# Kernel tuning notes

Measured on AMD Instinct MI355X. Metric: run time of the kernel, lower is better.

Reference implementation:

```python
import jax, jax.numpy as jnp
import numpy as np

N_NODES = 100000
N_EDGES = 3200000
IN_C = 128
OUT_C = 40
NEG_SLOPE = 0.2


def _p(key, shape, scale=0.1):
    return jax.random.normal(key, shape, dtype=jnp.float32) * scale


def setup_inputs() -> dict:
    key = jax.random.key(0)
    ks = jax.random.split(key, 16)
    x = jax.random.normal(ks[0], (N_NODES, IN_C), dtype=jnp.float32)
    edge_index = jax.random.randint(ks[1], (2, N_EDGES), 0, N_NODES, dtype=jnp.int32)
    # layer 1: in=128 -> heads=4, out=4 (concat -> 16)
    W1 = _p(ks[2], (IN_C, 4 * 4))
    a_src1 = _p(ks[3], (4, 4))
    a_dst1 = _p(ks[4], (4, 4))
    b1 = jnp.zeros((16,), jnp.float32)
    # layer 2: 16 -> heads=8, out=8 (concat -> 64)
    W2 = _p(ks[5], (16, 8 * 8))
    a_src2 = _p(ks[6], (8, 8))
    a_dst2 = _p(ks[7], (8, 8))
    b2 = jnp.zeros((64,), jnp.float32)
    # layer 3: 64 -> heads=1, out=OUT_C, concat=False
    W3 = _p(ks[8], (64, OUT_C))
    a_src3 = _p(ks[9], (1, OUT_C))
    a_dst3 = _p(ks[10], (1, OUT_C))
    b3 = jnp.zeros((OUT_C,), jnp.float32)
    return {"x": x, "edge_index": edge_index,
            "W1": W1, "a_src1": a_src1, "a_dst1": a_dst1, "b1": b1,
            "W2": W2, "a_src2": a_src2, "a_dst2": a_dst2, "b2": b2,
            "W3": W3, "a_src3": a_src3, "a_dst3": a_dst3, "b3": b3}


def gat_conv(x, src, dst, W, a_src, a_dst, b, heads, out_c, concat):
    # x: [N, F_in]; src/dst: [E] (self loops already included)
    N = x.shape[0]
    h = (x @ W).reshape(N, heads, out_c)                 # [N, H, C]
    e_src = jnp.sum(h * a_src, axis=-1)                  # [N, H]
    e_dst = jnp.sum(h * a_dst, axis=-1)                  # [N, H]
    e = jax.nn.leaky_relu(e_src[src] + e_dst[dst], NEG_SLOPE)  # [E, H]
    # segment softmax over edges grouped by destination node
    m = jax.ops.segment_max(e, dst, num_segments=N)      # [N, H]
    ex = jnp.exp(e - m[dst])
    s = jax.ops.segment_sum(ex, dst, num_segments=N)
    alpha = ex / (s[dst] + 1e-16)                        # [E, H]
    out = jax.ops.segment_sum(h[src] * alpha[:, :, None], dst, num_segments=N)  # [N, H, C]
    out = out.reshape(N, heads * out_c) if concat else out.mean(axis=1)
    return out + b


def reference(x, edge_index, W1, a_src1, a_dst1, b1, W2, a_src2, a_dst2, b2, W3, a_src3, a_dst3, b3):
    N = x.shape[0]
    loops = jnp.arange(N, dtype=edge_index.dtype)
    src = jnp.concatenate([edge_index[0], loops])
    dst = jnp.concatenate([edge_index[1], loops])
    h = jax.nn.elu(gat_conv(x, src, dst, W1, a_src1, a_dst1, b1, 4, 4, True))
    h = jax.nn.elu(gat_conv(h, src, dst, W2, a_src2, a_dst2, b2, 8, 8, True))
    out = gat_conv(h, src, dst, W3, a_src3, a_dst3, b3, 1, OUT_C, False)
    return out
```

## Files before the change

### kernel.cpp

```cpp
#include <hip/hip_runtime.h>

#define NN 100000
#define NE 3200000
#define ET (NE + NN)
#define NEG_SLOPE 0.2f
#define BSH 8
#define WIN (1 << BSH)
#define NBUC ((NN + WIN - 1) >> BSH)
#define NBLK 256
#define EPB ((ET + NBLK - 1) / NBLK)

__device__ __host__ __forceinline__ int swz(int b) {
    return (b & 7) * (NBLK / 8) + (b >> 3);
}

__device__ __forceinline__ float lrelu(float v) { return v > 0.f ? v : NEG_SLOPE * v; }

__device__ __forceinline__ unsigned short f2bf(float x) {
    unsigned u = __float_as_uint(x);
    return (unsigned short)((u + 0x7fffu + ((u >> 16) & 1u)) >> 16);
}
__device__ __forceinline__ float bflo(unsigned u) { return __uint_as_float(u << 16); }
__device__ __forceinline__ float bfhi(unsigned u) { return __uint_as_float(u & 0xffff0000u); }

typedef float f32x2 __attribute__((ext_vector_type(2)));
__device__ __forceinline__ f32x2 pkfma(f32x2 a, f32x2 b, f32x2 c) {
#if __has_builtin(__builtin_elementwise_fma)
    return __builtin_elementwise_fma(a, b, c);
#else
    f32x2 r; r.x = fmaf(a.x, b.x, c.x); r.y = fmaf(a.y, b.y, c.y); return r;
#endif
}
__device__ __forceinline__ f32x2 bfpair(unsigned u) {
    f32x2 r; r.x = bflo(u); r.y = bfhi(u); return r;
}


template <int FIN, int FOUT, int C>
__device__ __forceinline__ void gemm_attn_body(
    int idx, const float* __restrict__ x, const float* Ws,
    const float* __restrict__ a_src, const float* __restrict__ a_dst,
    unsigned short* __restrict__ h, float* __restrict__ esrc,
    float* __restrict__ edst, int N) {
    constexpr int HH = FOUT / C;
    constexpr int F4 = FOUT / 4;
    constexpr int TPH = C / 4;
    if (idx >= N * F4) return;
    int n = idx / F4, f4 = idx - n * F4;
    int fb = 4 * f4;
    const float4* xr = (const float4*)(x + (long)n * FIN);
    float a0 = 0.f, a1 = 0.f, a2 = 0.f, a3 = 0.f;
#pragma unroll
    for (int k4 = 0; k4 < FIN / 4; ++k4) {
        float4 xv = xr[k4];
        const float* wr = &Ws[(4 * k4) * FOUT + fb];
        float4 w0 = *(const float4*)(wr);
        float4 w1 = *(const float4*)(wr + FOUT);
        float4 w2 = *(const float4*)(wr + 2 * FOUT);
        float4 w3 = *(const float4*)(wr + 3 * FOUT);
        a0 = fmaf(xv.x, w0.x, a0); a1 = fmaf(xv.x, w0.y, a1);
        a2 = fmaf(xv.x, w0.z, a2); a3 = fmaf(xv.x, w0.w, a3);
        a0 = fmaf(xv.y, w1.x, a0); a1 = fmaf(xv.y, w1.y, a1);
        a2 = fmaf(xv.y, w1.z, a2); a3 = fmaf(xv.y, w1.w, a3);
        a0 = fmaf(xv.z, w2.x, a0); a1 = fmaf(xv.z, w2.y, a1);
        a2 = fmaf(xv.z, w2.z, a2); a3 = fmaf(xv.z, w2.w, a3);
        a0 = fmaf(xv.w, w3.x, a0); a1 = fmaf(xv.w, w3.y, a1);
        a2 = fmaf(xv.w, w3.z, a2); a3 = fmaf(xv.w, w3.w, a3);
    }
    unsigned short b0 = f2bf(a0), b1 = f2bf(a1), b2 = f2bf(a2), b3 = f2bf(a3);
    *(ushort4*)(h + (long)n * FOUT + fb) = make_ushort4(b0, b1, b2, b3);
    float q0 = bflo((unsigned)b0), q1 = bflo((unsigned)b1);
    float q2 = bflo((unsigned)b2), q3 = bflo((unsigned)b3);
    float vs = q0 * a_src[fb] + q1 * a_src[fb + 1] + q2 * a_src[fb + 2] + q3 * a_src[fb + 3];
    float vd = q0 * a_dst[fb] + q1 * a_dst[fb + 1] + q2 * a_dst[fb + 2] + q3 * a_dst[fb + 3];
#pragma unroll
    for (int o = 1; o < TPH; o <<= 1) {
        vs += __shfl_xor(vs, o);
        vd += __shfl_xor(vd, o);
    }
    if ((f4 % TPH) == 0) {
        int hh = f4 / TPH;
        esrc[n * HH + hh] = vs;
        edst[n * HH + hh] = vd;
    }
}


__global__ __launch_bounds__(256) void cntgemm_kernel(
    const int* __restrict__ dst, int* __restrict__ cnt,
    const float* __restrict__ x, const float* __restrict__ W,
    const float* __restrict__ a_src, const float* __restrict__ a_dst,
    unsigned short* __restrict__ h, float* __restrict__ esrc,
    float* __restrict__ edst, int N) {
    __shared__ __align__(16) char smem[128 * 16 * 4];
    if (blockIdx.x < NBLK) {
        int* hh = (int*)smem;
        for (int i = threadIdx.x; i < NBUC; i += 256) hh[i] = 0;
        __syncthreads();
        int lo = blockIdx.x * EPB;
        int hi = lo + EPB; if (hi > ET) hi = ET;
        for (int k = lo + threadIdx.x; k < hi; k += 256) {
            int d = (k < NE) ? dst[k] : k - NE;
            atomicAdd(&hh[d >> BSH], 1);
        }
        __syncthreads();
        int col = swz(blockIdx.x);
        for (int i = threadIdx.x; i < NBUC; i += 256)
            cnt[i * NBLK + col] = hh[i];
    } else {
        float* Ws = (float*)smem;
        for (int i = threadIdx.x; i < 128 * 16; i += 256) Ws[i] = W[i];
        __syncthreads();
        int idx = (blockIdx.x - NBLK) * 256 + threadIdx.x;
        gemm_attn_body<128, 16, 4>(idx, x, Ws, a_src, a_dst, h, esrc, edst, N);
    }
}


__global__ __launch_bounds__(256) void rowsum_kernel(const int* __restrict__ cnt,
                                                     int* __restrict__ tot) {
    int wave = threadIdx.x >> 6, lane = threadIdx.x & 63;
    int b = blockIdx.x * 4 + wave;
    if (b >= NBUC) return;
    int4 v = ((const int4*)(cnt + b * NBLK))[lane];
    int s = v.x + v.y + v.z + v.w;
#pragma unroll
    for (int off = 32; off; off >>= 1) s += __shfl_xor(s, off);
    if (lane == 0) tot[b] = s;
}

__global__ __launch_bounds__(1024) void scan_kernel(const int* __restrict__ tot,
                                                    int* __restrict__ bstart) {
    __shared__ int t[1024];
    int b = threadIdx.x;
    int s = (b < NBUC) ? tot[b] : 0;
    t[b] = s;
    __syncthreads();
    for (int off = 1; off < 1024; off <<= 1) {
        int v = (b >= off) ? t[b - off] : 0;
        __syncthreads();
        t[b] += v;
        __syncthreads();
    }
    if (b < NBUC) bstart[b] = t[b] - s;
    if (b == 0) bstart[NBUC] = ET;
}

__global__ __launch_bounds__(256) void base_kernel(int* __restrict__ cnt,
                                                   const int* __restrict__ bstart) {
    int wave = threadIdx.x >> 6, lane = threadIdx.x & 63;
    int b = blockIdx.x * 4 + wave;
    if (b >= NBUC) return;
    int run = bstart[b];
    for (int c0 = 0; c0 < NBLK; c0 += 64) {
        int v = cnt[b * NBLK + c0 + lane];
        int x = v;
#pragma unroll
        for (int off = 1; off < 64; off <<= 1) {
            int y = __shfl_up(x, off);
            if (lane >= off) x += y;
        }
        cnt[b * NBLK + c0 + lane] = run + x - v;
        run += __shfl(x, 63);
    }
}

__global__ __launch_bounds__(1024) void scatter_kernel(const int* __restrict__ src,
                                                       const int* __restrict__ dst,
                                                       const int* __restrict__ base,
                                                       unsigned* __restrict__ tmpp) {
    __shared__ int loff[NBUC];
    int col = swz(blockIdx.x);
    for (int i = threadIdx.x; i < NBUC; i += 1024) loff[i] = base[i * NBLK + col];
    __syncthreads();
    int lo = blockIdx.x * EPB;
    int hi = lo + EPB; if (hi > ET) hi = ET;
    for (int k = lo + threadIdx.x; k < hi; k += 1024) {
        int s, d;
        if (k < NE) { s = src[k]; d = dst[k]; }
        else { s = d = k - NE; }
        int p = atomicAdd(&loff[d >> BSH], 1);
        tmpp[p] = (unsigned)s | ((unsigned)(d & (WIN - 1)) << 17);
    }
}

__global__ __launch_bounds__(1024) void sort_kernel(const int* __restrict__ bstart,
                                                    const unsigned* __restrict__ tmpp,
                                                    int* __restrict__ rowptr,
                                                    int* __restrict__ ssrc) {
    __shared__ int histw[16][WIN];
    __shared__ int scan[WIN];
    __shared__ int cur[WIN];
    int buc = blockIdx.x;
    int nlo = buc << BSH;
    int nwin = NN - nlo; if (nwin > WIN) nwin = WIN;
    int lo = bstart[buc], hi = bstart[buc + 1];
    int tid = threadIdx.x;
    int wv = tid >> 6;
    for (int i = tid; i < 16 * WIN; i += 1024) ((int*)histw)[i] = 0;
    __syncthreads();
    for (int k = lo + tid; k < hi; k += 1024)
        atomicAdd(&histw[wv][tmpp[k] >> 17], 1);
    __syncthreads();
    int myh = 0;
    if (tid < WIN) {
        int s = 0;
#pragma unroll
        for (int w = 0; w < 16; ++w) s += histw[w][tid];
        myh = s;
        scan[tid] = s;
    }
    __syncthreads();
    for (int off = 1; off < WIN; off <<= 1) {
        int v = (tid >= off && tid < WIN) ? scan[tid - off] : 0;
        __syncthreads();
        if (tid < WIN) scan[tid] += v;
        __syncthreads();
    }
    if (tid < WIN) {
        int ex = scan[tid] - myh;
        cur[tid] = ex;
        if (tid < nwin) rowptr[nlo + tid] = lo + ex;
    }
    if (buc == 0 && tid == 0) rowptr[NN] = ET;
    __syncthreads();
    for (int k = lo + tid; k < hi; k += 1024) {
        unsigned e = tmpp[k];
        int p = atomicAdd(&cur[e >> 17], 1);
        ssrc[lo + p] = (int)(e & 0x1FFFFu);
    }
}


template <int FIN, int FOUT, int C>
__global__ __launch_bounds__(256) void gemm_attn_kernel(
    const float* __restrict__ x, const float* __restrict__ W,
    const float* __restrict__ a_src, const float* __restrict__ a_dst,
    unsigned short* __restrict__ h, float* __restrict__ esrc,
    float* __restrict__ edst, int N) {
    __shared__ __align__(16) float Ws[FIN * FOUT];
    for (int i = threadIdx.x; i < FIN * FOUT; i += blockDim.x) Ws[i] = W[i];
    __syncthreads();
    int idx = blockIdx.x * blockDim.x + threadIdx.x;
    gemm_attn_body<FIN, FOUT, C>(idx, x, Ws, a_src, a_dst, h, esrc, edst, N);
}

__global__ __launch_bounds__(320) void gemm_attn3_kernel(
    const float* __restrict__ x, const float* __restrict__ W,
    const float* __restrict__ a_src, const float* __restrict__ a_dst,
    unsigned short* __restrict__ h, float* __restrict__ esrc,
    float* __restrict__ edst, int N) {
    constexpr int FIN = 64, FOUT = 40, F4 = 10;
    __shared__ __align__(16) float Ws[FIN * FOUT];
    __shared__ float ps[320], pd[320];
    int tid = threadIdx.x;
    for (int i = tid; i < FIN * FOUT; i += 320) Ws[i] = W[i];
    __syncthreads();
    int idx = blockIdx.x * 320 + tid;
    int n = idx / F4, f4 = idx - n * F4;
    float vs = 0.f, vd = 0.f;
    if (n < N) {
        int fb = 4 * f4;
        const float4* xr = (const float4*)(x + (long)n * FIN);
        float a0 = 0.f, a1 = 0.f, a2 = 0.f, a3 = 0.f;
#pragma unroll
        for (int k4 = 0; k4 < FIN / 4; ++k4) {
            float4 xv = xr[k4];
            const float* wr = &Ws[(4 * k4) * FOUT + fb];
            float4 w0 = *(const float4*)(wr);
            float4 w1 = *(const float4*)(wr + FOUT);
            float4 w2 = *(const float4*)(wr + 2 * FOUT);
            float4 w3 = *(const float4*)(wr + 3 * FOUT);
            a0 = fmaf(xv.x, w0.x, a0); a1 = fmaf(xv.x, w0.y, a1);
            a2 = fmaf(xv.x, w0.z, a2); a3 = fmaf(xv.x, w0.w, a3);
            a0 = fmaf(xv.y, w1.x, a0); a1 = fmaf(xv.y, w1.y, a1);
            a2 = fmaf(xv.y, w1.z, a2); a3 = fmaf(xv.y, w1.w, a3);
            a0 = fmaf(xv.z, w2.x, a0); a1 = fmaf(xv.z, w2.y, a1);
            a2 = fmaf(xv.z, w2.z, a2); a3 = fmaf(xv.z, w2.w, a3);
            a0 = fmaf(xv.w, w3.x, a0); a1 = fmaf(xv.w, w3.y, a1);
            a2 = fmaf(xv.w, w3.z, a2); a3 = fmaf(xv.w, w3.w, a3);
        }
        unsigned short b0 = f2bf(a0), b1 = f2bf(a1), b2 = f2bf(a2), b3 = f2bf(a3);
        *(ushort4*)(h + (long)n * FOUT + fb) = make_ushort4(b0, b1, b2, b3);
        float q0 = bflo((unsigned)b0), q1 = bflo((unsigned)b1);
        float q2 = bflo((unsigned)b2), q3 = bflo((unsigned)b3);
        vs = q0 * a_src[fb] + q1 * a_src[fb + 1] + q2 * a_src[fb + 2] + q3 * a_src[fb + 3];
        vd = q0 * a_dst[fb] + q1 * a_dst[fb + 1] + q2 * a_dst[fb + 2] + q3 * a_dst[fb + 3];
    }
    ps[tid] = vs; pd[tid] = vd;
    __syncthreads();
    if (tid < 32) {
        int n0 = blockIdx.x * 32 + tid;
        if (n0 < N) {
            float s = 0.f, d = 0.f;
#pragma unroll
            for (int j = 0; j < F4; ++j) { s += ps[tid * F4 + j]; d += pd[tid * F4 + j]; }
            esrc[n0] = s;
            edst[n0] = d;
        }
    }
}

template <int H, int C, int L, int G, int NPW, int FPL, int RSL, int U, bool ELU>
__device__ __forceinline__ void agg_body(
    const int* __restrict__ rowptr, const int* __restrict__ ssrc,
    const float* __restrict__ esrc, const float* __restrict__ edst,
    const unsigned short* __restrict__ hbuf, const float* __restrict__ b,
    float* __restrict__ out, int N) {
    constexpr int F = H * C;
    constexpr int AQ = (F + FPL - 1) / FPL;
    constexpr int S = L * G;
    constexpr int P = FPL / 2;
    static_assert(S * NPW == 64, "wave layout");
    static_assert(AQ <= L, "lanes cover features");
    int lane = threadIdx.x & 63;
    int wave = threadIdx.x >> 6;
    int sub = lane / S;
    int ls = lane - sub * S;
    int g = ls / L, q = ls - g * L;
    int n = (blockIdx.x * 4 + wave) * NPW + sub;
    if (n >= N) return;
    const bool act = (q < AQ);
    int h = act ? (FPL * q) / C : 0;
    int qa = act ? q : 0;
    float edn = edst[n * H + h];
    int beg = rowptr[n], end = rowptr[n + 1];
    int kend = end - 1;
    float sum = 0.f;
    f32x2 acc[P];
#pragma unroll
    for (int i = 0; i < P; ++i) { acc[i].x = 0.f; acc[i].y = 0.f; }

    int k = beg + g;
    int ss[U];
#pragma unroll
    for (int u = 0; u < U; ++u) {
        int kk = k + u * G;
        ss[u] = ssrc[kk < kend ? kk : kend];
    }
    while (k < end) {
        uint4 hv4[U];
        uint2 hv2[U];
        float es[U];
#pragma unroll
        for (int u = 0; u < U; ++u) {
            if constexpr (FPL == 8) hv4[u] = ((const uint4*)hbuf)[ss[u] * RSL + qa];
            else hv2[u] = ((const uint2*)hbuf)[ss[u] * RSL + qa];
            es[u] = esrc[ss[u] * H + h];
        }
        int kn = k + U * G;
        int sn[U];
#pragma unroll
        for (int u = 0; u < U; ++u) {
            int kk = kn + u * G;
            sn[u] = ssrc[kk < kend ? kk : kend];
        }
        __builtin_amdgcn_sched_barrier(0);
#pragma unroll
        for (int u = 0; u < U; ++u) {
            float ex = (act && (k + u * G < end)) ? __expf(lrelu(es[u] + edn)) : 0.f;
            f32x2 exv; exv.x = ex; exv.y = ex;
            if constexpr (FPL == 8) {
                uint4 v = hv4[u];
                acc[0] = pkfma(exv, bfpair(v.x), acc[0]);
                acc[1] = pkfma(exv, bfpair(v.y), acc[1]);
                acc[2] = pkfma(exv, bfpair(v.z), acc[2]);
                acc[3] = pkfma(exv, bfpair(v.w), acc[3]);
            } else {
                uint2 v = hv2[u];
                acc[0] = pkfma(exv, bfpair(v.x), acc[0]);
                acc[1] = pkfma(exv, bfpair(v.y), acc[1]);
            }
            sum += ex;
        }
#pragma unroll
        for (int u = 0; u < U; ++u) ss[u] = sn[u];
        k = kn;
    }
#pragma unroll
    for (int step = L; step < S; step <<= 1) {
        sum += __shfl_xor(sum, step);
#pragma unroll
        for (int i = 0; i < P; ++i) {
            acc[i].x += __shfl_xor(acc[i].x, step);
            acc[i].y += __shfl_xor(acc[i].y, step);
        }
    }
    if (g == 0 && act) {
        float inv = 1.f / (sum + 1e-16f);
        float v[FPL];
#pragma unroll
        for (int i = 0; i < FPL; ++i) {
            float av = (i & 1) ? acc[i >> 1].y : acc[i >> 1].x;
            v[i] = av * inv + b[FPL * q + i];
            if (ELU) v[i] = v[i] > 0.f ? v[i] : __expf(v[i]) - 1.f;
        }
        float* op = out + n * F + FPL * q;
#pragma unroll
        for (int i = 0; i < FPL; i += 4)
            *(float4*)(op + i) = make_float4(v[i], v[i + 1], v[i + 2], v[i + 3]);
    }
}

__global__ __launch_bounds__(256) void agg1_kernel(
    const int* __restrict__ rowptr, const int* __restrict__ ssrc,
    const float* __restrict__ esrc, const float* __restrict__ edst,
    const unsigned short* __restrict__ hbuf, const float* __restrict__ b,
    float* __restrict__ out, int N) {
    agg_body<4, 4, 4, 8, 2, 4, 4, 5, true>(rowptr, ssrc, esrc, edst, hbuf, b, out, N);
}
__global__ __launch_bounds__(256) void agg2_kernel(
    const int* __restrict__ rowptr, const int* __restrict__ ssrc,
    const float* __restrict__ esrc, const float* __restrict__ edst,
    const unsigned short* __restrict__ hbuf, const float* __restrict__ b,
    float* __restrict__ out, int N) {
    agg_body<8, 8, 8, 8, 1, 8, 8, 5, true>(rowptr, ssrc, esrc, edst, hbuf, b, out, N);
}
__global__ __launch_bounds__(256) void agg3_kernel(
    const int* __restrict__ rowptr, const int* __restrict__ ssrc,
    const float* __restrict__ esrc, const float* __restrict__ edst,
    const unsigned short* __restrict__ hbuf, const float* __restrict__ b,
    float* __restrict__ out, int N) {
    agg_body<1, 40, 8, 8, 1, 8, 5, 5, false>(rowptr, ssrc, esrc, edst, hbuf, b, out, N);
}

static inline int cdiv(long a, int b) { return (int)((a + b - 1) / b); }

extern "C" void kernel_launch(void* const* d_in, const int* in_sizes, int n_in,
                              void* d_out, int out_size, void* d_ws, size_t ws_size,
                              hipStream_t stream) {
    const float* x1 = (const float*)d_in[0];
    const int* ei = (const int*)d_in[1];
    const int* src = ei;
    const int* dst = ei + NE;
    const float* W1 = (const float*)d_in[2];
    const float* as1 = (const float*)d_in[3];
    const float* ad1 = (const float*)d_in[4];
    const float* b1 = (const float*)d_in[5];
    const float* W2 = (const float*)d_in[6];
    const float* as2 = (const float*)d_in[7];
    const float* ad2 = (const float*)d_in[8];
    const float* b2 = (const float*)d_in[9];
    const float* W3 = (const float*)d_in[10];
    const float* as3 = (const float*)d_in[11];
    const float* ad3 = (const float*)d_in[12];
    const float* b3 = (const float*)d_in[13];
    float* out = (float*)d_out;

    char* wsb = (char*)d_ws;
    unsigned short* hbuf = (unsigned short*)wsb;  wsb += (long)NN * 64 * 2;
    float* x2 = (float*)wsb;         wsb += (long)NN * 16 * 4;
    float* x3 = (float*)wsb;         wsb += (long)NN * 64 * 4;
    float* esrc = (float*)wsb;       wsb += (long)NN * 8 * 4;
    float* edst = (float*)wsb;       wsb += (long)NN * 8 * 4;
    unsigned* tmpp = (unsigned*)wsb; wsb += (long)ET * 4;
    int* ssrc = (int*)wsb;           wsb += (long)ET * 4;
    int* rowptr = (int*)wsb;         wsb += (long)(NN + 1) * 4;
    int* cnt = (int*)wsb;            wsb += (long)NBUC * NBLK * 4;
    int* bstart = (int*)wsb;         wsb += (long)(NBUC + 1) * 4;
    int* tot = (int*)wsb;            wsb += (long)NBUC * 4;

    const int B = 256;

    cntgemm_kernel<<<NBLK + cdiv((long)NN * 4, B), B, 0, stream>>>(
        dst, cnt, x1, W1, as1, ad1, hbuf, esrc, edst, NN);
    rowsum_kernel<<<cdiv(NBUC, 4), B, 0, stream>>>(cnt, tot);
    scan_kernel<<<1, 1024, 0, stream>>>(tot, bstart);
    base_kernel<<<cdiv(NBUC, 4), B, 0, stream>>>(cnt, bstart);
    scatter_kernel<<<NBLK, 1024, 0, stream>>>(src, dst, cnt, tmpp);
    sort_kernel<<<NBUC, 1024, 0, stream>>>(bstart, tmpp, rowptr, ssrc);

    agg1_kernel<<<cdiv(NN, 8), B, 0, stream>>>(
        rowptr, ssrc, esrc, edst, hbuf, b1, x2, NN);

    gemm_attn_kernel<16, 64, 8><<<cdiv((long)NN * 16, B), B, 0, stream>>>(
        x2, W2, as2, ad2, hbuf, esrc, edst, NN);
    agg2_kernel<<<cdiv(NN, 4), B, 0, stream>>>(
        rowptr, ssrc, esrc, edst, hbuf, b2, x3, NN);

    gemm_attn3_kernel<<<cdiv(NN, 32), 320, 0, stream>>>(
        x3, W3, as3, ad3, hbuf, esrc, edst, NN);
    agg3_kernel<<<cdiv(NN, 4), B, 0, stream>>>(
        rowptr, ssrc, esrc, edst, hbuf, b3, out, NN);
}
```

Baseline: 420.6 us.

## Split layer-3 features into 64B-aligned and tail buffers; fuse scan into base kernel

The layer-3 bf16 features (40 per node, 80 bytes per row) are split into a 32-feature buffer with 64-byte rows and an 8-feature tail buffer, so the per-edge gathers in agg3 line up better with cache lines. The aggregation picks which table and stride to use per lane. Separately, the single-block scan kernel is merged into base_kernel: each block redundantly scans the bucket totals in shared memory, which removes one launch. The cost is a little redundant scan work per block, plus extra pointer selection in the gather path.

```diff
diff --git a/kernel.cpp b/kernel.cpp
--- a/kernel.cpp
+++ b/kernel.cpp
@@ -129,29 +129,31 @@
     if (lane == 0) tot[b] = s;
 }
 
-__global__ __launch_bounds__(1024) void scan_kernel(const int* __restrict__ tot,
-                                                    int* __restrict__ bstart) {
-    __shared__ int t[1024];
-    int b = threadIdx.x;
-    int s = (b < NBUC) ? tot[b] : 0;
-    t[b] = s;
-    __syncthreads();
-    for (int off = 1; off < 1024; off <<= 1) {
-        int v = (b >= off) ? t[b - off] : 0;
-        __syncthreads();
-        t[b] += v;
-        __syncthreads();
-    }
-    if (b < NBUC) bstart[b] = t[b] - s;
-    if (b == 0) bstart[NBUC] = ET;
-}
-
-__global__ __launch_bounds__(256) void base_kernel(int* __restrict__ cnt,
-                                                   const int* __restrict__ bstart) {
-    int wave = threadIdx.x >> 6, lane = threadIdx.x & 63;
-    int b = blockIdx.x * 4 + wave;
+__global__ __launch_bounds__(512) void base_kernel(int* __restrict__ cnt,
+                                                   const int* __restrict__ tot,
+                                                   int* __restrict__ bstart) {
+    __shared__ int t[512];
+    __shared__ int ex[512];
+    int tid = threadIdx.x;
+    int s = (tid < NBUC) ? tot[tid] : 0;
+    t[tid] = s;
+    __syncthreads();
+    for (int off = 1; off < 512; off <<= 1) {
+        int v = (tid >= off) ? t[tid - off] : 0;
+        __syncthreads();
+        t[tid] += v;
+        __syncthreads();
+    }
+    ex[tid] = t[tid] - s;
+    __syncthreads();
+    if (blockIdx.x == 0) {
+        if (tid < NBUC) bstart[tid] = ex[tid];
+        if (tid == 0) bstart[NBUC] = ET;
+    }
+    int wave = tid >> 6, lane = tid & 63;
+    int b = blockIdx.x * 8 + wave;
     if (b >= NBUC) return;
-    int run = bstart[b];
+    int run = ex[b];
     for (int c0 = 0; c0 < NBLK; c0 += 64) {
         int v = cnt[b * NBLK + c0 + lane];
         int x = v;
@@ -218,9 +220,9 @@
         __syncthreads();
     }
     if (tid < WIN) {
-        int ex = scan[tid] - myh;
-        cur[tid] = ex;
-        if (tid < nwin) rowptr[nlo + tid] = lo + ex;
+        int exl = scan[tid] - myh;
+        cur[tid] = exl;
+        if (tid < nwin) rowptr[nlo + tid] = lo + exl;
     }
     if (buc == 0 && tid == 0) rowptr[NN] = ET;
     __syncthreads();
@@ -248,8 +250,8 @@
 __global__ __launch_bounds__(320) void gemm_attn3_kernel(
     const float* __restrict__ x, const float* __restrict__ W,
     const float* __restrict__ a_src, const float* __restrict__ a_dst,
-    unsigned short* __restrict__ h, float* __restrict__ esrc,
-    float* __restrict__ edst, int N) {
+    unsigned short* __restrict__ hA, unsigned short* __restrict__ hB,
+    float* __restrict__ esrc, float* __restrict__ edst, int N) {
     constexpr int FIN = 64, FOUT = 40, F4 = 10;
     __shared__ __align__(16) float Ws[FIN * FOUT];
     __shared__ float ps[320], pd[320];
@@ -281,7 +283,10 @@
             a2 = fmaf(xv.w, w3.z, a2); a3 = fmaf(xv.w, w3.w, a3);
         }
         unsigned short b0 = f2bf(a0), b1 = f2bf(a1), b2 = f2bf(a2), b3 = f2bf(a3);
-        *(ushort4*)(h + (long)n * FOUT + fb) = make_ushort4(b0, b1, b2, b3);
+        if (f4 < 8)
+            *(ushort4*)(hA + (long)n * 32 + fb) = make_ushort4(b0, b1, b2, b3);
+        else
+            *(ushort4*)(hB + (long)n * 8 + (fb - 32)) = make_ushort4(b0, b1, b2, b3);
         float q0 = bflo((unsigned)b0), q1 = bflo((unsigned)b1);
         float q2 = bflo((unsigned)b2), q3 = bflo((unsigned)b3);
         vs = q0 * a_src[fb] + q1 * a_src[fb + 1] + q2 * a_src[fb + 2] + q3 * a_src[fb + 3];
@@ -301,12 +306,12 @@
     }
 }
 
-template <int H, int C, int L, int G, int NPW, int FPL, int RSL, int U, bool ELU>
+template <int H, int C, int L, int G, int NPW, int FPL, int RSL, int U, bool ELU, int SPLIT>
 __device__ __forceinline__ void agg_body(
     const int* __restrict__ rowptr, const int* __restrict__ ssrc,
     const float* __restrict__ esrc, const float* __restrict__ edst,
-    const unsigned short* __restrict__ hbuf, const float* __restrict__ b,
-    float* __restrict__ out, int N) {
+    const unsigned short* __restrict__ hbuf, const unsigned short* __restrict__ hbuf2,
+    const float* __restrict__ b, float* __restrict__ out, int N) {
     constexpr int F = H * C;
     constexpr int AQ = (F + FPL - 1) / FPL;
     constexpr int S = L * G;
@@ -323,6 +328,21 @@
     const bool act = (q < AQ);
     int h = act ? (FPL * q) / C : 0;
     int qa = act ? q : 0;
+    const uint4* tbl4;
+    const uint2* tbl2;
+    int rmul, roff;
+    if constexpr (SPLIT) {
+        bool inA = (qa < RSL);
+        tbl4 = inA ? (const uint4*)hbuf : (const uint4*)hbuf2;
+        rmul = inA ? RSL : 1;
+        roff = inA ? qa : 0;
+        tbl2 = (const uint2*)hbuf;
+    } else {
+        tbl4 = (const uint4*)hbuf;
+        tbl2 = (const uint2*)hbuf;
+        rmul = RSL;
+        roff = qa;
+    }
     float edn = edst[n * H + h];
     int beg = rowptr[n], end = rowptr[n + 1];
     int kend = end - 1;
@@ -344,8 +364,8 @@
         float es[U];
 #pragma unroll
         for (int u = 0; u < U; ++u) {
-            if constexpr (FPL == 8) hv4[u] = ((const uint4*)hbuf)[ss[u] * RSL + qa];
-            else hv2[u] = ((const uint2*)hbuf)[ss[u] * RSL + qa];
+            if constexpr (FPL == 8) hv4[u] = tbl4[ss[u] * rmul + roff];
+            else hv2[u] = tbl2[ss[u] * RSL + qa];
             es[u] = esrc[ss[u] * H + h];
         }
         int kn = k + U * G;
@@ -407,21 +427,21 @@
     const float* __restrict__ esrc, const float* __restrict__ edst,
     const unsigned short* __restrict__ hbuf, const float* __restrict__ b,
     float* __restrict__ out, int N) {
-    agg_body<4, 4, 4, 8, 2, 4, 4, 5, true>(rowptr, ssrc, esrc, edst, hbuf, b, out, N);
+    agg_body<4, 4, 4, 8, 2, 4, 4, 5, true, 0>(rowptr, ssrc, esrc, edst, hbuf, hbuf, b, out, N);
 }
 __global__ __launch_bounds__(256) void agg2_kernel(
     const int* __restrict__ rowptr, const int* __restrict__ ssrc,
     const float* __restrict__ esrc, const float* __restrict__ edst,
     const unsigned short* __restrict__ hbuf, const float* __restrict__ b,
     float* __restrict__ out, int N) {
-    agg_body<8, 8, 8, 8, 1, 8, 8, 5, true>(rowptr, ssrc, esrc, edst, hbuf, b, out, N);
+    agg_body<8, 8, 8, 8, 1, 8, 8, 5, true, 0>(rowptr, ssrc, esrc, edst, hbuf, hbuf, b, out, N);
 }
 __global__ __launch_bounds__(256) void agg3_kernel(
     const int* __restrict__ rowptr, const int* __restrict__ ssrc,
     const float* __restrict__ esrc, const float* __restrict__ edst,
-    const unsigned short* __restrict__ hbuf, const float* __restrict__ b,
-    float* __restrict__ out, int N) {
-    agg_body<1, 40, 8, 8, 1, 8, 5, 5, false>(rowptr, ssrc, esrc, edst, hbuf, b, out, N);
+    const unsigned short* __restrict__ hA, const unsigned short* __restrict__ hB,
+    const float* __restrict__ b, float* __restrict__ out, int N) {
+    agg_body<1, 40, 8, 8, 1, 8, 4, 5, false, 1>(rowptr, ssrc, esrc, edst, hA, hB, b, out, N);
 }
 
 static inline int cdiv(long a, int b) { return (int)((a + b - 1) / b); }
@@ -449,6 +469,7 @@
 
     char* wsb = (char*)d_ws;
     unsigned short* hbuf = (unsigned short*)wsb;  wsb += (long)NN * 64 * 2;
+    unsigned short* hbufB = (unsigned short*)wsb; wsb += (long)NN * 8 * 2;
     float* x2 = (float*)wsb;         wsb += (long)NN * 16 * 4;
     float* x3 = (float*)wsb;         wsb += (long)NN * 64 * 4;
     float* esrc = (float*)wsb;       wsb += (long)NN * 8 * 4;
@@ -465,8 +486,7 @@
     cntgemm_kernel<<<NBLK + cdiv((long)NN * 4, B), B, 0, stream>>>(
         dst, cnt, x1, W1, as1, ad1, hbuf, esrc, edst, NN);
     rowsum_kernel<<<cdiv(NBUC, 4), B, 0, stream>>>(cnt, tot);
-    scan_kernel<<<1, 1024, 0, stream>>>(tot, bstart);
-    base_kernel<<<cdiv(NBUC, 4), B, 0, stream>>>(cnt, bstart);
+    base_kernel<<<cdiv(NBUC, 8), 512, 0, stream>>>(cnt, tot, bstart);
     scatter_kernel<<<NBLK, 1024, 0, stream>>>(src, dst, cnt, tmpp);
     sort_kernel<<<NBUC, 1024, 0, stream>>>(bstart, tmpp, rowptr, ssrc);
 
@@ -479,7 +499,7 @@
         rowptr, ssrc, esrc, edst, hbuf, b2, x3, NN);
 
     gemm_attn3_kernel<<<cdiv(NN, 32), 320, 0, stream>>>(
-        x3, W3, as3, ad3, hbuf, esrc, edst, NN);
+        x3, W3, as3, ad3, hbuf, hbufB, esrc, edst, NN);
     agg3_kernel<<<cdiv(NN, 4), B, 0, stream>>>(
-        rowptr, ssrc, esrc, edst, hbuf, b3, out, NN);
-}
+        rowptr, ssrc, esrc, edst, hbuf, hbufB, b3, out, NN);
+}
```

After: 429.7 us. +2.2%, slower.
